# Performance work log

Measured on AMD Instinct MI355X. Metric: run time of the kernel, lower is better.

## Reference

```python
import jax, jax.numpy as jnp
import numpy as np

N, E, F_IN, H, C = 100000, 1600000, 128, 128, 40

def setup_inputs() -> dict:
    key = jax.random.key(0)
    ks = jax.random.split(key, 8)
    s = 0.05  # param init scale
    return {
        "x": jax.random.normal(ks[0], (N, F_IN), dtype=jnp.float32),
        "edge_index": jax.random.randint(ks[1], (2, E), 0, N, dtype=jnp.int64),
        "W1_rel": jax.random.normal(ks[2], (H, F_IN), dtype=jnp.float32) * s,
        "b1": jnp.zeros((H,), dtype=jnp.float32),
        "W1_root": jax.random.normal(ks[3], (H, F_IN), dtype=jnp.float32) * s,
        "W2_rel": jax.random.normal(ks[4], (C, H), dtype=jnp.float32) * s,
        "b2": jnp.zeros((C,), dtype=jnp.float32),
        "W2_root": jax.random.normal(ks[5], (C, H), dtype=jnp.float32) * s,
    }

def _graph_conv(x, src, dst, W_rel, b, W_root, n_nodes):
    # PyG GraphConv: lin_rel(sum_{j in N(i)} x_j) + lin_root(x_i); lin_root has no bias
    agg = jax.ops.segment_sum(x[src], dst, num_segments=n_nodes)  # [N, F]
    return agg @ W_rel.T + b + x @ W_root.T

def reference(x, edge_index, W1_rel, b1, W1_root, W2_rel, b2, W2_root):
    src, dst = edge_index[0], edge_index[1]
    h = _graph_conv(x, src, dst, W1_rel, b1, W1_root, N)
    h = jax.nn.relu(h)  # dropout is identity in eval mode
    out = _graph_conv(h, src, dst, W2_rel, b2, W2_root, N)
    return jax.nn.log_softmax(out, axis=1)
```

## Files before the change

kernel.cpp:

```cpp
#include <hip/hip_runtime.h>
#include <hip/hip_bf16.h>
#include <math.h>

typedef __bf16 bf16x8 __attribute__((ext_vector_type(8)));
typedef float f32x4 __attribute__((ext_vector_type(4)));
typedef float f32x2 __attribute__((ext_vector_type(2)));
typedef unsigned int uint32;

#define CHUNK 8192
#define MAXBINS 512

__device__ __forceinline__ float bflo(uint32 u) { return __uint_as_float(u << 16); }
__device__ __forceinline__ float bfhi(uint32 u) { return __uint_as_float(u & 0xffff0000u); }
__device__ __forceinline__ unsigned short tobf(float f) {
    return __builtin_bit_cast(unsigned short, __float2bfloat16(f));
}
__device__ __forceinline__ unsigned char tofp8(float f) {
    return (unsigned char)(__builtin_amdgcn_cvt_pk_fp8_f32(f, f, 0, false) & 0xff);
}


__global__ __launch_bounds__(256) void binhist_kernel(
    const int* __restrict__ dst, int* __restrict__ blkhist,
    int nE, int nChunks, int nBins)
{
    __shared__ int h[MAXBINS];
    int blk = blockIdx.x, t = threadIdx.x;
    for (int i = t; i < nBins; i += 256) h[i] = 0;
    __syncthreads();
    int e0 = blk * CHUNK;
    int e1 = e0 + CHUNK; if (e1 > nE) e1 = nE;
    for (int e = e0 + t; e < e1; e += 256)
        atomicAdd(&h[dst[e] >> 8], 1);
    __syncthreads();
    for (int b = t; b < nBins; b += 256)
        blkhist[(size_t)b * nChunks + blk] = h[b];
}

__global__ __launch_bounds__(256) void csr_partial_kernel(
    const int* __restrict__ cnt, int* __restrict__ blocksum, int nN)
{
    int b = blockIdx.x, t = threadIdx.x;
    int base = b * 1024 + t * 4;
    int s = 0;
    #pragma unroll
    for (int k = 0; k < 4; ++k) { int i = base + k; if (i < nN) s += cnt[i]; }
    #pragma unroll
    for (int off = 1; off < 64; off <<= 1) s += __shfl_xor(s, off);
    __shared__ int ws[4];
    int lane = t & 63, w = t >> 6;
    if (lane == 0) ws[w] = s;
    __syncthreads();
    if (t == 0) blocksum[b] = ws[0] + ws[1] + ws[2] + ws[3];
}

__global__ __launch_bounds__(1024) void csr_scanblocks_kernel(
    const int* __restrict__ blocksum, int* __restrict__ blockpre,
    int nB, int* __restrict__ outtot, int nN)
{
    __shared__ int sm[1024];
    int t = threadIdx.x;
    int v = (t < nB) ? blocksum[t] : 0;
    sm[t] = v;
    __syncthreads();
    for (int off = 1; off < 1024; off <<= 1) {
        int u = (t >= off) ? sm[t - off] : 0;
        __syncthreads();
        sm[t] += u;
        __syncthreads();
    }
    if (t < nB) blockpre[t] = sm[t] - v;
    if (t == 1023) outtot[nN] = sm[1023];
}

__global__ __launch_bounds__(256) void csr_scanfinal_kernel(
    const int* __restrict__ cnt, const int* __restrict__ blockpre,
    int* __restrict__ out, int nN)
{
    int b = blockIdx.x, t = threadIdx.x;
    int base = b * 1024 + t * 4;
    int c[4]; int s = 0;
    #pragma unroll
    for (int k = 0; k < 4; ++k) { int i = base + k; c[k] = (i < nN) ? cnt[i] : 0; s += c[k]; }
    int lane = t & 63, w = t >> 6;
    int inc = s;
    #pragma unroll
    for (int off = 1; off < 64; off <<= 1) {
        int u = __shfl_up(inc, off);
        if (lane >= off) inc += u;
    }
    __shared__ int ws[4];
    if (lane == 63) ws[w] = inc;
    __syncthreads();
    int wpre = 0;
    for (int i = 0; i < w; ++i) wpre += ws[i];
    int run = blockpre[b] + wpre + (inc - s);
    #pragma unroll
    for (int k = 0; k < 4; ++k) {
        int i = base + k;
        if (i < nN) { out[i] = run; run += c[k]; }
    }
}

__global__ __launch_bounds__(256) void binscatter_kernel(
    const int* __restrict__ src, const int* __restrict__ dst,
    const int* __restrict__ blkbase, uint32* __restrict__ packed,
    int nE, int nChunks, int nBins)
{
    __shared__ int h[MAXBINS];
    int blk = blockIdx.x, t = threadIdx.x;
    for (int i = t; i < nBins; i += 256) h[i] = 0;
    __syncthreads();
    int e0 = blk * CHUNK;
    int e1 = e0 + CHUNK; if (e1 > nE) e1 = nE;
    for (int e = e0 + t; e < e1; e += 256) {
        int d = dst[e];
        int b = d >> 8;
        int r = atomicAdd(&h[b], 1);
        int pos = blkbase[(size_t)b * nChunks + blk] + r;
        packed[pos] = (uint32)src[e] | ((uint32)(d & 255) << 24);
    }
}

__global__ __launch_bounds__(256) void binsort_kernel(
    const uint32* __restrict__ packed, const int* __restrict__ blkbase,
    int* __restrict__ rowptr, int* __restrict__ sorted_src,
    int nChunks, int nBins, int nN, int nE)
{
    __shared__ int h[256];
    __shared__ int offs[256];
    __shared__ int ws[4];
    int b = blockIdx.x, t = threadIdx.x;
    int segbase = blkbase[(size_t)b * nChunks];
    int segend  = (b + 1 < nBins) ? blkbase[(size_t)(b + 1) * nChunks] : nE;

    h[t] = 0;
    __syncthreads();
    for (int i = segbase + t; i < segend; i += 256)
        atomicAdd(&h[packed[i] >> 24], 1);
    __syncthreads();

    int c = h[t];
    int lane = t & 63, w = t >> 6;
    int inc = c;
    #pragma unroll
    for (int off = 1; off < 64; off <<= 1) {
        int u = __shfl_up(inc, off);
        if (lane >= off) inc += u;
    }
    if (lane == 63) ws[w] = inc;
    __syncthreads();
    int wpre = 0;
    for (int i = 0; i < w; ++i) wpre += ws[i];
    int ex = wpre + inc - c;
    offs[t] = ex;
    int node = b * 256 + t;
    if (node < nN) rowptr[node] = segbase + ex;
    if (b == 0 && t == 0) rowptr[nN] = nE;
    __syncthreads();

    for (int i = segbase + t; i < segend; i += 256) {
        uint32 pk = packed[i];
        int ld = (int)(pk >> 24);
        int r = atomicAdd(&offs[ld], 1);
        sorted_src[segbase + r] = (int)(pk & 0x00FFFFFFu);
    }
}


__global__ __launch_bounds__(256) void cvt_fp8_kernel(
    const float4* __restrict__ in, uint32* __restrict__ out, int n4)
{
    int i = blockIdx.x * blockDim.x + threadIdx.x;
    int stride = gridDim.x * blockDim.x;
    for (; i < n4; i += stride) {
        float4 v = in[i];
        int w = __builtin_amdgcn_cvt_pk_fp8_f32(v.x, v.y, 0, false);
        w = __builtin_amdgcn_cvt_pk_fp8_f32(v.z, v.w, w, true);
        out[i] = (uint32)w;
    }
}

__global__ __launch_bounds__(256) void prep_weights_kernel(
    const float* __restrict__ W1_rel, const float* __restrict__ W1_root,
    const float* __restrict__ W2_rel, const float* __restrict__ W2_root,
    unsigned short* __restrict__ W1relB, unsigned short* __restrict__ W1rootB,
    unsigned short* __restrict__ Wpq)
{
    int i = blockIdx.x * 256 + threadIdx.x;
    if (i < 16384) {
        W1relB[i] = tobf(W1_rel[i]);
    } else if (i < 32768) {
        int j = i - 16384;
        W1rootB[j] = tobf(W1_root[j]);
    } else if (i < 32768 + 10240) {
        int j = i - 32768;
        int o = j >> 7, k = j & 127;
        float v = (o < 40) ? W2_rel[o * 128 + k] : W2_root[(o - 40) * 128 + k];
        Wpq[j] = tobf(v);
    }
}

__global__ __launch_bounds__(256) void aggregate_fp8_kernel(
    const uint32* __restrict__ xf8u,
    const int* __restrict__ rowptr,
    const int* __restrict__ sorted_src,
    uint2* __restrict__ aggout2,
    int nN)
{
    int wave = threadIdx.x >> 6;
    int lane = threadIdx.x & 63;
    int node = blockIdx.x * 4 + wave;
    if (node >= nN) return;
    int half = lane >> 5, l32 = lane & 31;
    int beg = rowptr[node], end = rowptr[node + 1];
    float a0 = 0.f, a1 = 0.f, a2 = 0.f, a3 = 0.f;
    int j = beg;
    for (; j + 8 <= end; j += 8) {
        uint32 u0 = xf8u[(size_t)sorted_src[j + half] * 32 + l32];
        uint32 u1 = xf8u[(size_t)sorted_src[j + 2 + half] * 32 + l32];
        uint32 u2 = xf8u[(size_t)sorted_src[j + 4 + half] * 32 + l32];
        uint32 u3 = xf8u[(size_t)sorted_src[j + 6 + half] * 32 + l32];
        f32x2 p0 = __builtin_amdgcn_cvt_pk_f32_fp8(u0, false);
        f32x2 q0 = __builtin_amdgcn_cvt_pk_f32_fp8(u0, true);
        f32x2 p1 = __builtin_amdgcn_cvt_pk_f32_fp8(u1, false);
        f32x2 q1 = __builtin_amdgcn_cvt_pk_f32_fp8(u1, true);
        f32x2 p2 = __builtin_amdgcn_cvt_pk_f32_fp8(u2, false);
        f32x2 q2 = __builtin_amdgcn_cvt_pk_f32_fp8(u2, true);
        f32x2 p3 = __builtin_amdgcn_cvt_pk_f32_fp8(u3, false);
        f32x2 q3 = __builtin_amdgcn_cvt_pk_f32_fp8(u3, true);
        a0 += (p0[0] + p1[0]) + (p2[0] + p3[0]);
        a1 += (p0[1] + p1[1]) + (p2[1] + p3[1]);
        a2 += (q0[0] + q1[0]) + (q2[0] + q3[0]);
        a3 += (q0[1] + q1[1]) + (q2[1] + q3[1]);
    }
    for (; j + 2 <= end; j += 2) {
        uint32 u = xf8u[(size_t)sorted_src[j + half] * 32 + l32];
        f32x2 p0 = __builtin_amdgcn_cvt_pk_f32_fp8(u, false);
        f32x2 p1 = __builtin_amdgcn_cvt_pk_f32_fp8(u, true);
        a0 += p0[0]; a1 += p0[1]; a2 += p1[0]; a3 += p1[1];
    }
    if (j < end && half == 0) {
        uint32 u = xf8u[(size_t)sorted_src[j] * 32 + l32];
        f32x2 p0 = __builtin_amdgcn_cvt_pk_f32_fp8(u, false);
        f32x2 p1 = __builtin_amdgcn_cvt_pk_f32_fp8(u, true);
        a0 += p0[0]; a1 += p0[1]; a2 += p1[0]; a3 += p1[1];
    }
    a0 += __shfl_xor(a0, 32);
    a1 += __shfl_xor(a1, 32);
    a2 += __shfl_xor(a2, 32);
    a3 += __shfl_xor(a3, 32);
    if (half == 0) {
        uint2 o;
        o.x = (uint32)tobf(a0) | ((uint32)tobf(a1) << 16);
        o.y = (uint32)tobf(a2) | ((uint32)tobf(a3) << 16);
        aggout2[(size_t)node * 32 + l32] = o;
    }
}

__global__ __launch_bounds__(256) void gemm_fused_kernel(
    const unsigned short* __restrict__ aggb,
    const float* __restrict__ xf,
    const unsigned short* __restrict__ Wrel,
    const unsigned short* __restrict__ Wroot,
    const unsigned short* __restrict__ Wpq,
    const float* __restrict__ b1,
    unsigned char* __restrict__ pf8,
    unsigned short* __restrict__ qb,
    int nN)
{
    __shared__ __align__(16) unsigned char lds[32768];
    __shared__ __align__(16) unsigned char hlds[16384];
    int tid = threadIdx.x;
    int wave = tid >> 6, lane = tid & 63;
    int i0 = blockIdx.x * 64 + wave * 16;
    int mrow = lane & 15, kslot = lane >> 4;
    int arow = i0 + mrow; if (arow >= nN) arow = 0;

    f32x4 acc[8] = {};
    const unsigned short* Wsrc[2] = {Wrel, Wroot};

    for (int ph = 0; ph < 2; ++ph) {
        __syncthreads();
        const uint4* src = (const uint4*)Wsrc[ph];
        for (int c = tid; c < 2048; c += 256) {
            int row = c >> 4;
            int off = (c & 15) << 4;
            *(uint4*)(&lds[row * 256 + (off ^ ((row & 7) << 4))]) = src[c];
        }
        __syncthreads();
        if (ph == 0) {
            const unsigned short* Ap = aggb + (size_t)arow * 128 + kslot * 8;
            #pragma unroll
            for (int t = 0; t < 4; ++t) {
                bf16x8 a = *(const bf16x8*)(Ap + t * 32);
                #pragma unroll
                for (int ct = 0; ct < 8; ++ct) {
                    int o = ct * 16 + mrow;
                    int off = (t * 64 + kslot * 16) ^ ((o & 7) << 4);
                    bf16x8 b = *(const bf16x8*)(&lds[o * 256 + off]);
                    acc[ct] = __builtin_amdgcn_mfma_f32_16x16x32_bf16(a, b, acc[ct], 0, 0, 0);
                }
            }
        } else {
            const float* Ap = xf + (size_t)arow * 128 + kslot * 8;
            #pragma unroll
            for (int t = 0; t < 4; ++t) {
                float4 f0 = *(const float4*)(Ap + t * 32);
                float4 f1 = *(const float4*)(Ap + t * 32 + 4);
                union { bf16x8 v; unsigned short u[8]; } a;
                a.u[0] = tobf(f0.x); a.u[1] = tobf(f0.y);
                a.u[2] = tobf(f0.z); a.u[3] = tobf(f0.w);
                a.u[4] = tobf(f1.x); a.u[5] = tobf(f1.y);
                a.u[6] = tobf(f1.z); a.u[7] = tobf(f1.w);
                #pragma unroll
                for (int ct = 0; ct < 8; ++ct) {
                    int o = ct * 16 + mrow;
                    int off = (t * 64 + kslot * 16) ^ ((o & 7) << 4);
                    bf16x8 b = *(const bf16x8*)(&lds[o * 256 + off]);
                    acc[ct] = __builtin_amdgcn_mfma_f32_16x16x32_bf16(a.v, b, acc[ct], 0, 0, 0);
                }
            }
        }
    }

    #pragma unroll
    for (int ct = 0; ct < 8; ++ct) {
        int col = ct * 16 + mrow;
        float bias = b1[col];
        #pragma unroll
        for (int r = 0; r < 4; ++r) {
            int rl = wave * 16 + kslot * 4 + r;
            float v = fmaxf(acc[ct][r] + bias, 0.f);
            *(unsigned short*)(&hlds[rl * 256 + ((col * 2) ^ ((rl & 7) << 4))]) = tobf(v);
        }
    }
    __syncthreads();

    {
        const uint4* src = (const uint4*)Wpq;
        for (int c = tid; c < 1280; c += 256) {
            int row = c >> 4;
            int off = (c & 15) << 4;
            *(uint4*)(&lds[row * 256 + (off ^ ((row & 7) << 4))]) = src[c];
        }
    }
    __syncthreads();

    f32x4 acc2[5] = {};
    {
        int rl = wave * 16 + mrow;
        #pragma unroll
        for (int t = 0; t < 4; ++t) {
            bf16x8 a = *(const bf16x8*)(&hlds[rl * 256 + ((t * 64 + kslot * 16) ^ ((rl & 7) << 4))]);
            #pragma unroll
            for (int ct = 0; ct < 5; ++ct) {
                int o = ct * 16 + mrow;
                int off = (t * 64 + kslot * 16) ^ ((o & 7) << 4);
                bf16x8 b = *(const bf16x8*)(&lds[o * 256 + off]);
                acc2[ct] = __builtin_amdgcn_mfma_f32_16x16x32_bf16(a, b, acc2[ct], 0, 0, 0);
            }
        }
    }

    #pragma unroll
    for (int ct = 0; ct < 5; ++ct) {
        int col = ct * 16 + mrow;
        #pragma unroll
        for (int r = 0; r < 4; ++r) {
            int row = i0 + kslot * 4 + r;
            if (row < nN) {
                if (col < 40) pf8[(size_t)row * 40 + col] = tofp8(acc2[ct][r]);
                else          qb[(size_t)row * 40 + (col - 40)] = tobf(acc2[ct][r]);
            }
        }
    }
}

__global__ __launch_bounds__(256) void final_lsm_kernel(
    const unsigned short* __restrict__ pf8u,
    const uint32* __restrict__ qbu,
    const int* __restrict__ rowptr,
    const int* __restrict__ sorted_src,
    const float* __restrict__ b2,
    float* __restrict__ out,
    int nN)
{
    int wave = threadIdx.x >> 6;
    int lane = threadIdx.x & 63;
    int node = blockIdx.x * 4 + wave;
    if (node >= nN) return;

    int esub = (lane >= 40) ? 2 : (lane >= 20 ? 1 : 0);
    int cp   = lane - esub * 20;
    bool active = lane < 60;
    int beg = rowptr[node], end = rowptr[node + 1];

    float a0 = 0.f, a1 = 0.f;
    int j = beg;
    if (active) {
        for (; j + 9 <= end; j += 9) {
            int s0 = sorted_src[j + esub];
            int s1 = sorted_src[j + 3 + esub];
            int s2 = sorted_src[j + 6 + esub];
            uint32 u0 = pf8u[(size_t)s0 * 20 + cp];
            uint32 u1 = pf8u[(size_t)s1 * 20 + cp];
            uint32 u2 = pf8u[(size_t)s2 * 20 + cp];
            f32x2 p0 = __builtin_amdgcn_cvt_pk_f32_fp8(u0, false);
            f32x2 p1 = __builtin_amdgcn_cvt_pk_f32_fp8(u1, false);
            f32x2 p2 = __builtin_amdgcn_cvt_pk_f32_fp8(u2, false);
            a0 += (p0[0] + p1[0]) + p2[0];
            a1 += (p0[1] + p1[1]) + p2[1];
        }
        for (; j + 3 <= end; j += 3) {
            uint32 u = pf8u[(size_t)sorted_src[j + esub] * 20 + cp];
            f32x2 p = __builtin_amdgcn_cvt_pk_f32_fp8(u, false);
            a0 += p[0]; a1 += p[1];
        }
        int rem = end - j;
        if (esub < rem) {
            uint32 u = pf8u[(size_t)sorted_src[j + esub] * 20 + cp];
            f32x2 p = __builtin_amdgcn_cvt_pk_f32_fp8(u, false);
            a0 += p[0]; a1 += p[1];
        }
    }
    {
        float t0 = __shfl(a0, cp + 20), t1 = __shfl(a0, cp + 40);
        float t2 = __shfl(a1, cp + 20), t3 = __shfl(a1, cp + 40);
        a0 += t0 + t1;
        a1 += t2 + t3;
    }

    float v0, v1;
    if (lane < 20) {
        uint32 uq = qbu[(size_t)node * 20 + lane];
        float2 bb = *(const float2*)(b2 + 2 * lane);
        v0 = a0 + bflo(uq) + bb.x;
        v1 = a1 + bfhi(uq) + bb.y;
    } else {
        v0 = v1 = -INFINITY;
    }

    float m = fmaxf(v0, v1);
    #pragma unroll
    for (int off = 32; off >= 1; off >>= 1) m = fmaxf(m, __shfl_xor(m, off));
    float s = (lane < 20) ? (expf(v0 - m) + expf(v1 - m)) : 0.f;
    #pragma unroll
    for (int off = 32; off >= 1; off >>= 1) s += __shfl_xor(s, off);
    float lse = m + logf(s);

    if (lane < 20) {
        float2 o = make_float2(v0 - lse, v1 - lse);
        *(float2*)(out + (size_t)node * 40 + 2 * lane) = o;
    }
}


static inline char* alignup(char* p, size_t a) {
    return (char*)(((uintptr_t)p + a - 1) & ~(uintptr_t)(a - 1));
}

extern "C" void kernel_launch(void* const* d_in, const int* in_sizes, int n_in,
                              void* d_out, int out_size, void* d_ws, size_t ws_size,
                              hipStream_t stream)
{
    const float* x       = (const float*)d_in[0];
    const int*   ei      = (const int*)d_in[1];
    const float* W1_rel  = (const float*)d_in[2];
    const float* b1      = (const float*)d_in[3];
    const float* W1_root = (const float*)d_in[4];
    const float* W2_rel  = (const float*)d_in[5];
    const float* b2      = (const float*)d_in[6];
    const float* W2_root = (const float*)d_in[7];

    int N = in_sizes[0] / 128;
    int E = in_sizes[1] / 2;
    const int* srcp = ei;
    const int* dstp = ei + E;

    int nChunks = (E + CHUNK - 1) / CHUNK;
    int nBins   = (N + 255) >> 8;
    int nScan   = nBins * nChunks;
    int nB2     = (nScan + 1023) / 1024;
    size_t nf = (size_t)N * 128;

    char* p = (char*)d_ws;
    unsigned char*  xf8     = (unsigned char*)p;   p += nf;
    unsigned short* aggb    = (unsigned short*)p;  p += nf * 2;
    p = alignup(p, 16);
    unsigned short* qb      = (unsigned short*)p;  p += (size_t)N * 40 * 2;
    p = alignup(p, 16);
    unsigned char*  pf8     = (unsigned char*)p;   p += (size_t)N * 40 + 64;
    p = alignup(p, 16);
    unsigned short* W1relB  = (unsigned short*)p;  p += 16384 * 2;
    unsigned short* W1rootB = (unsigned short*)p;  p += 16384 * 2;
    unsigned short* Wpq     = (unsigned short*)p;  p += 10240 * 2;
    p = alignup(p, 16);
    int* rowptr     = (int*)p;  p += (size_t)(N + 1) * 4;
    p = alignup(p, 16);
    int* blkhist    = (int*)p;  p += (size_t)nScan * 4;
    int* blkbase    = (int*)p;  p += (size_t)(nScan + 1) * 4;
    int* blocksum   = (int*)p;  p += (size_t)nB2 * 4;
    int* blockpre   = (int*)p;  p += (size_t)nB2 * 4;
    p = alignup(p, 16);
    uint32* packed  = (uint32*)p; p += (size_t)E * 4;
    p = alignup(p, 16);
    int* sorted_src = (int*)p;  p += (size_t)E * 4;

    if ((size_t)(p - (char*)d_ws) > ws_size || nBins > MAXBINS) return;

    binhist_kernel<<<nChunks, 256, 0, stream>>>(dstp, blkhist, E, nChunks, nBins);
    csr_partial_kernel<<<nB2, 256, 0, stream>>>(blkhist, blocksum, nScan);
    csr_scanblocks_kernel<<<1, 1024, 0, stream>>>(blocksum, blockpre, nB2, blkbase, nScan);
    csr_scanfinal_kernel<<<nB2, 256, 0, stream>>>(blkhist, blockpre, blkbase, nScan);
    binscatter_kernel<<<nChunks, 256, 0, stream>>>(srcp, dstp, blkbase, packed, E, nChunks, nBins);
    binsort_kernel<<<nBins, 256, 0, stream>>>(packed, blkbase, rowptr, sorted_src,
                                              nChunks, nBins, N, E);

    cvt_fp8_kernel<<<2048, 256, 0, stream>>>((const float4*)x, (uint32*)xf8, (int)(nf / 4));
    prep_weights_kernel<<<(43008 + 255) / 256, 256, 0, stream>>>(
        W1_rel, W1_root, W2_rel, W2_root, W1relB, W1rootB, Wpq);

    aggregate_fp8_kernel<<<(N + 3) / 4, 256, 0, stream>>>(
        (const uint32*)xf8, rowptr, sorted_src, (uint2*)aggb, N);

    gemm_fused_kernel<<<(N + 63) / 64, 256, 0, stream>>>(
        aggb, x, W1relB, W1rootB, Wpq, b1, pf8, qb, N);

    final_lsm_kernel<<<(N + 3) / 4, 256, 0, stream>>>(
        (const unsigned short*)pf8, (const uint32*)qb, rowptr, sorted_src,
        b2, (float*)d_out, N);
}
```

Measured before the change: 203.5 us.

## Merge prep kernels, unroll aggregation, pad pf8 rows, halve CSR chunk

Merges the fp8 conversion of x and the weight conversion into one launch, which removes a kernel launch. Adds a 16-edge unrolled loop in the first aggregation to keep more gathers in flight. Pads the fp8 layer-2 projection rows from 40 to 64 bytes so each row gather is 64-byte aligned. Halves the CSR build chunk size, giving more histogram blocks but a larger scan. The padding uses more memory and bandwidth for pf8 writes, and the bigger unroll raises register pressure.

```diff
diff --git a/kernel.cpp b/kernel.cpp
--- a/kernel.cpp
+++ b/kernel.cpp
@@ -7,7 +7,7 @@
 typedef float f32x2 __attribute__((ext_vector_type(2)));
 typedef unsigned int uint32;
 
-#define CHUNK 8192
+#define CHUNK 4096
 #define MAXBINS 512
 
 __device__ __forceinline__ float bflo(uint32 u) { return __uint_as_float(u << 16); }
@@ -167,37 +167,35 @@
     }
 }
 
-
-__global__ __launch_bounds__(256) void cvt_fp8_kernel(
-    const float4* __restrict__ in, uint32* __restrict__ out, int n4)
-{
-    int i = blockIdx.x * blockDim.x + threadIdx.x;
-    int stride = gridDim.x * blockDim.x;
-    for (; i < n4; i += stride) {
-        float4 v = in[i];
-        int w = __builtin_amdgcn_cvt_pk_fp8_f32(v.x, v.y, 0, false);
-        w = __builtin_amdgcn_cvt_pk_fp8_f32(v.z, v.w, w, true);
-        out[i] = (uint32)w;
-    }
-}
-
-__global__ __launch_bounds__(256) void prep_weights_kernel(
+__global__ __launch_bounds__(256) void prep_all_kernel(
+    const float4* __restrict__ xin, uint32* __restrict__ xf8out, int n4,
     const float* __restrict__ W1_rel, const float* __restrict__ W1_root,
     const float* __restrict__ W2_rel, const float* __restrict__ W2_root,
     unsigned short* __restrict__ W1relB, unsigned short* __restrict__ W1rootB,
     unsigned short* __restrict__ Wpq)
 {
-    int i = blockIdx.x * 256 + threadIdx.x;
-    if (i < 16384) {
-        W1relB[i] = tobf(W1_rel[i]);
-    } else if (i < 32768) {
-        int j = i - 16384;
-        W1rootB[j] = tobf(W1_root[j]);
-    } else if (i < 32768 + 10240) {
-        int j = i - 32768;
-        int o = j >> 7, k = j & 127;
-        float v = (o < 40) ? W2_rel[o * 128 + k] : W2_root[(o - 40) * 128 + k];
-        Wpq[j] = tobf(v);
+    if (blockIdx.x < 168) {
+        int i = blockIdx.x * 256 + threadIdx.x;
+        if (i < 16384) {
+            W1relB[i] = tobf(W1_rel[i]);
+        } else if (i < 32768) {
+            int j = i - 16384;
+            W1rootB[j] = tobf(W1_root[j]);
+        } else if (i < 32768 + 10240) {
+            int j = i - 32768;
+            int o = j >> 7, k = j & 127;
+            float v = (o < 40) ? W2_rel[o * 128 + k] : W2_root[(o - 40) * 128 + k];
+            Wpq[j] = tobf(v);
+        }
+    } else {
+        int i = (blockIdx.x - 168) * 256 + threadIdx.x;
+        int stride = (gridDim.x - 168) * 256;
+        for (; i < n4; i += stride) {
+            float4 v = xin[i];
+            int w = __builtin_amdgcn_cvt_pk_fp8_f32(v.x, v.y, 0, false);
+            w = __builtin_amdgcn_cvt_pk_fp8_f32(v.z, v.w, w, true);
+            xf8out[i] = (uint32)w;
+        }
     }
 }
 
@@ -216,6 +214,36 @@
     int beg = rowptr[node], end = rowptr[node + 1];
     float a0 = 0.f, a1 = 0.f, a2 = 0.f, a3 = 0.f;
     int j = beg;
+    for (; j + 16 <= end; j += 16) {
+        uint32 u0 = xf8u[(size_t)sorted_src[j + half] * 32 + l32];
+        uint32 u1 = xf8u[(size_t)sorted_src[j + 2 + half] * 32 + l32];
+        uint32 u2 = xf8u[(size_t)sorted_src[j + 4 + half] * 32 + l32];
+        uint32 u3 = xf8u[(size_t)sorted_src[j + 6 + half] * 32 + l32];
+        uint32 u4 = xf8u[(size_t)sorted_src[j + 8 + half] * 32 + l32];
+        uint32 u5 = xf8u[(size_t)sorted_src[j + 10 + half] * 32 + l32];
+        uint32 u6 = xf8u[(size_t)sorted_src[j + 12 + half] * 32 + l32];
+        uint32 u7 = xf8u[(size_t)sorted_src[j + 14 + half] * 32 + l32];
+        f32x2 p0 = __builtin_amdgcn_cvt_pk_f32_fp8(u0, false);
+        f32x2 q0 = __builtin_amdgcn_cvt_pk_f32_fp8(u0, true);
+        f32x2 p1 = __builtin_amdgcn_cvt_pk_f32_fp8(u1, false);
+        f32x2 q1 = __builtin_amdgcn_cvt_pk_f32_fp8(u1, true);
+        f32x2 p2 = __builtin_amdgcn_cvt_pk_f32_fp8(u2, false);
+        f32x2 q2 = __builtin_amdgcn_cvt_pk_f32_fp8(u2, true);
+        f32x2 p3 = __builtin_amdgcn_cvt_pk_f32_fp8(u3, false);
+        f32x2 q3 = __builtin_amdgcn_cvt_pk_f32_fp8(u3, true);
+        f32x2 p4 = __builtin_amdgcn_cvt_pk_f32_fp8(u4, false);
+        f32x2 q4 = __builtin_amdgcn_cvt_pk_f32_fp8(u4, true);
+        f32x2 p5 = __builtin_amdgcn_cvt_pk_f32_fp8(u5, false);
+        f32x2 q5 = __builtin_amdgcn_cvt_pk_f32_fp8(u5, true);
+        f32x2 p6 = __builtin_amdgcn_cvt_pk_f32_fp8(u6, false);
+        f32x2 q6 = __builtin_amdgcn_cvt_pk_f32_fp8(u6, true);
+        f32x2 p7 = __builtin_amdgcn_cvt_pk_f32_fp8(u7, false);
+        f32x2 q7 = __builtin_amdgcn_cvt_pk_f32_fp8(u7, true);
+        a0 += ((p0[0] + p1[0]) + (p2[0] + p3[0])) + ((p4[0] + p5[0]) + (p6[0] + p7[0]));
+        a1 += ((p0[1] + p1[1]) + (p2[1] + p3[1])) + ((p4[1] + p5[1]) + (p6[1] + p7[1]));
+        a2 += ((q0[0] + q1[0]) + (q2[0] + q3[0])) + ((q4[0] + q5[0]) + (q6[0] + q7[0]));
+        a3 += ((q0[1] + q1[1]) + (q2[1] + q3[1])) + ((q4[1] + q5[1]) + (q6[1] + q7[1]));
+    }
     for (; j + 8 <= end; j += 8) {
         uint32 u0 = xf8u[(size_t)sorted_src[j + half] * 32 + l32];
         uint32 u1 = xf8u[(size_t)sorted_src[j + 2 + half] * 32 + l32];
@@ -370,7 +398,7 @@
         for (int r = 0; r < 4; ++r) {
             int row = i0 + kslot * 4 + r;
             if (row < nN) {
-                if (col < 40) pf8[(size_t)row * 40 + col] = tofp8(acc2[ct][r]);
+                if (col < 40) pf8[(size_t)row * 64 + col] = tofp8(acc2[ct][r]);
                 else          qb[(size_t)row * 40 + (col - 40)] = tobf(acc2[ct][r]);
             }
         }
@@ -403,9 +431,9 @@
             int s0 = sorted_src[j + esub];
             int s1 = sorted_src[j + 3 + esub];
             int s2 = sorted_src[j + 6 + esub];
-            uint32 u0 = pf8u[(size_t)s0 * 20 + cp];
-            uint32 u1 = pf8u[(size_t)s1 * 20 + cp];
-            uint32 u2 = pf8u[(size_t)s2 * 20 + cp];
+            uint32 u0 = pf8u[(size_t)s0 * 32 + cp];
+            uint32 u1 = pf8u[(size_t)s1 * 32 + cp];
+            uint32 u2 = pf8u[(size_t)s2 * 32 + cp];
             f32x2 p0 = __builtin_amdgcn_cvt_pk_f32_fp8(u0, false);
             f32x2 p1 = __builtin_amdgcn_cvt_pk_f32_fp8(u1, false);
             f32x2 p2 = __builtin_amdgcn_cvt_pk_f32_fp8(u2, false);
@@ -413,13 +441,13 @@
             a1 += (p0[1] + p1[1]) + p2[1];
         }
         for (; j + 3 <= end; j += 3) {
-            uint32 u = pf8u[(size_t)sorted_src[j + esub] * 20 + cp];
+            uint32 u = pf8u[(size_t)sorted_src[j + esub] * 32 + cp];
             f32x2 p = __builtin_amdgcn_cvt_pk_f32_fp8(u, false);
             a0 += p[0]; a1 += p[1];
         }
         int rem = end - j;
         if (esub < rem) {
-            uint32 u = pf8u[(size_t)sorted_src[j + esub] * 20 + cp];
+            uint32 u = pf8u[(size_t)sorted_src[j + esub] * 32 + cp];
             f32x2 p = __builtin_amdgcn_cvt_pk_f32_fp8(u, false);
             a0 += p[0]; a1 += p[1];
         }
@@ -487,10 +515,10 @@
     char* p = (char*)d_ws;
     unsigned char*  xf8     = (unsigned char*)p;   p += nf;
     unsigned short* aggb    = (unsigned short*)p;  p += nf * 2;
+    p = alignup(p, 64);
+    unsigned char*  pf8     = (unsigned char*)p;   p += (size_t)N * 64;
     p = alignup(p, 16);
     unsigned short* qb      = (unsigned short*)p;  p += (size_t)N * 40 * 2;
-    p = alignup(p, 16);
-    unsigned char*  pf8     = (unsigned char*)p;   p += (size_t)N * 40 + 64;
     p = alignup(p, 16);
     unsigned short* W1relB  = (unsigned short*)p;  p += 16384 * 2;
     unsigned short* W1rootB = (unsigned short*)p;  p += 16384 * 2;
@@ -517,8 +545,8 @@
     binsort_kernel<<<nBins, 256, 0, stream>>>(packed, blkbase, rowptr, sorted_src,
                                               nChunks, nBins, N, E);
 
-    cvt_fp8_kernel<<<2048, 256, 0, stream>>>((const float4*)x, (uint32*)xf8, (int)(nf / 4));
-    prep_weights_kernel<<<(43008 + 255) / 256, 256, 0, stream>>>(
+    prep_all_kernel<<<168 + 2048, 256, 0, stream>>>(
+        (const float4*)x, (uint32*)xf8, (int)(nf / 4),
         W1_rel, W1_root, W2_rel, W2_root, W1relB, W1rootB, Wpq);
 
     aggregate_fp8_kernel<<<(N + 3) / 4, 256, 0, stream>>>(
```

Measured after the change: 196.1 us. 3.7% less time.
